# Optimization experiments

Measured on AMD Instinct MI355X. Metric: run time of the kernel, lower is better.

## Reference

```python
import jax, jax.numpy as jnp
import numpy as np

B, N, DIM = 4, 4096, 1024
HEADS, DFF, WIN = 16, 4096, 128
EPS = 1e-5


def _layernorm(x, w, b):
    mu = jnp.mean(x, axis=-1, keepdims=True)
    var = jnp.mean(jnp.square(x - mu), axis=-1, keepdims=True)
    return (x - mu) * jax.lax.rsqrt(var + EPS) * w + b


def _local_attention(q, k, v, window):
    # q,k,v: (B, h, N, d); non-causal, look_backward=1, look_forward=1
    Bq, h, n, d = q.shape
    nb = n // window
    scale = d ** -0.5
    q = q.reshape(Bq * h, nb, window, d) * scale
    k = k.reshape(Bq * h, nb, window, d)
    v = v.reshape(Bq * h, nb, window, d)

    def look_around(t):  # (BH, nb, w, d) -> (BH, nb, 3w, d)
        tp = jnp.pad(t, ((0, 0), (1, 1), (0, 0), (0, 0)))
        return jnp.concatenate([tp[:, :-2], tp[:, 1:-1], tp[:, 2:]], axis=2)

    kk = look_around(k)
    vv = look_around(v)

    # validity mask for out-of-range look-around buckets
    idx = jnp.arange(n).reshape(nb, window)
    idx_p = jnp.pad(idx, ((1, 1), (0, 0)), constant_values=-1)
    kidx = jnp.concatenate([idx_p[:-2], idx_p[1:-1], idx_p[2:]], axis=1)  # (nb, 3w)
    valid = (kidx >= 0)[None, :, None, :]  # (1, nb, 1, 3w)

    sim = jnp.einsum('bnid,bnjd->bnij', q, kk)  # (BH, nb, w, 3w)
    neg = jnp.finfo(sim.dtype).min
    sim = jnp.where(valid, sim, neg)
    attn = jax.nn.softmax(sim, axis=-1)
    out = jnp.einsum('bnij,bnjd->bnid', attn, vv)
    return out.reshape(Bq, h, n, d)


def setup_inputs() -> dict:
    key = jax.random.key(0)
    ks = jax.random.split(key, 8)
    w = lambda k, shape: jax.random.normal(k, shape, jnp.float32) * 0.02
    return {
        'x': jax.random.normal(ks[0], (B, N, DIM), jnp.float32),
        'ln1_w': jnp.ones((DIM,), jnp.float32), 'ln1_b': jnp.zeros((DIM,), jnp.float32),
        'qkv_w': w(ks[1], (3 * DIM, DIM)), 'qkv_b': jnp.zeros((3 * DIM,), jnp.float32),
        'proj_w': w(ks[2], (DIM, DIM)), 'proj_b': jnp.zeros((DIM,), jnp.float32),
        'ln2_w': jnp.ones((DIM,), jnp.float32), 'ln2_b': jnp.zeros((DIM,), jnp.float32),
        'fc1_w': w(ks[3], (DFF, DIM)), 'fc1_b': jnp.zeros((DFF,), jnp.float32),
        'fc2_w': w(ks[4], (DIM, DFF)), 'fc2_b': jnp.zeros((DIM,), jnp.float32),
    }


def reference(x, ln1_w, ln1_b, qkv_w, qkv_b, proj_w, proj_b, ln2_w, ln2_b, fc1_w, fc1_b, fc2_w, fc2_b):
    Bx, n, C = x.shape
    h = HEADS
    hd = C // h
    x_norm = _layernorm(x, ln1_w, ln1_b)
    qkv = x_norm @ qkv_w.T + qkv_b  # (B, N, 3C)
    qkv = qkv.reshape(Bx, n, 3, h, hd).transpose(2, 0, 3, 1, 4)  # (3, B, h, N, hd)
    q, k, v = qkv[0], qkv[1], qkv[2]
    attn_out = _local_attention(q, k, v, WIN)  # (B, h, N, hd)
    attn_out = attn_out.transpose(0, 2, 1, 3).reshape(Bx, n, C)
    x = x + (attn_out @ proj_w.T + proj_b)
    y = _layernorm(x, ln2_w, ln2_b)
    y = jax.nn.gelu(y @ fc1_w.T + fc1_b, approximate=False)
    x = x + (y @ fc2_w.T + fc2_b)
    return x
```

## Files before the change

kernel.cpp:

```cpp
#include <hip/hip_runtime.h>
#include <math.h>

typedef unsigned short u16;
typedef __attribute__((ext_vector_type(4))) float f32x4;
typedef __attribute__((ext_vector_type(8))) __bf16 bf16x8;
typedef __attribute__((ext_vector_type(8))) u16 u16x8;
typedef __attribute__((ext_vector_type(4))) u16 u16x4;

__device__ __forceinline__ float bf2f(u16 v) {
    unsigned int u = ((unsigned int)v) << 16;
    return __builtin_bit_cast(float, u);
}
__device__ __forceinline__ u16 f2bf(float f) {
    unsigned int x = __builtin_bit_cast(unsigned int, f);
    x += 0x7fffu + ((x >> 16) & 1u);
    return (u16)(x >> 16);
}

__device__ __forceinline__ void load_lds16(const u16* g, u16* l) {
    __builtin_amdgcn_global_load_lds((const __attribute__((address_space(1))) void*)g,
                                     (__attribute__((address_space(3))) void*)l, 16, 0, 0);
}

__global__ __launch_bounds__(256) void cvt_kernel(const float* __restrict__ in,
                                                  u16* __restrict__ out, int n)
{
    const int i = (blockIdx.x * 256 + threadIdx.x) * 4;
    if (i >= n) return;
    const float4 f = *(const float4*)(in + i);
    u16x4 o;
    o[0] = f2bf(f.x); o[1] = f2bf(f.y); o[2] = f2bf(f.z); o[3] = f2bf(f.w);
    *(u16x4*)(out + i) = o;
}

template<int EPI, int RES, bool OF32>
__global__ __launch_bounds__(256) void gemm_bt(
    const u16* __restrict__ A, const u16* __restrict__ W,
    const float* __restrict__ bias,
    const float* __restrict__ resf, const u16* __restrict__ resb,
    void* __restrict__ O0v, u16* __restrict__ O1, u16* __restrict__ O2,
    int M, int N, int K, int mbase)
{
    __shared__ u16 As[128 * 32];
    __shared__ u16 Bs[128 * 32];
    const int tid  = threadIdx.x;
    const int wave = tid >> 6;
    const int lane = tid & 63;
    const int m0   = blockIdx.y * 128;
    const int n0   = blockIdx.x * 128;
    const int wm   = (wave >> 1) * 64;
    const int wn   = (wave & 1) * 64;

    const int srow = lane >> 2;
    const int scol = (lane & 3) * 8;
    const u16* ag0 = A + (size_t)(m0 + wave * 16 + srow) * K + scol;
    const u16* ag1 = ag0 + (size_t)64 * K;
    const u16* bg0 = W + (size_t)(n0 + wave * 16 + srow) * K + scol;
    const u16* bg1 = bg0 + (size_t)64 * K;
    u16* as0 = As + (wave * 16) * 32;
    u16* as1 = As + (64 + wave * 16) * 32;
    u16* bs0 = Bs + (wave * 16) * 32;
    u16* bs1 = Bs + (64 + wave * 16) * 32;

    const int colq = lane & 15;
    const int quad = lane >> 4;

    f32x4 acc[4][4] = {};

    for (int k0 = 0; k0 < K; k0 += 32) {
        if (k0) __syncthreads();
        load_lds16(ag0 + k0, as0);
        load_lds16(ag1 + k0, as1);
        load_lds16(bg0 + k0, bs0);
        load_lds16(bg1 + k0, bs1);
        __syncthreads();
        bf16x8 a[4], b[4];
#pragma unroll
        for (int i = 0; i < 4; ++i) {
            a[i] = *(const bf16x8*)(As + (wm + i * 16 + colq) * 32 + quad * 8);
            b[i] = *(const bf16x8*)(Bs + (wn + i * 16 + colq) * 32 + quad * 8);
        }
#pragma unroll
        for (int mi = 0; mi < 4; ++mi)
#pragma unroll
            for (int ni = 0; ni < 4; ++ni)
                acc[mi][ni] = __builtin_amdgcn_mfma_f32_16x16x32_bf16(a[mi], b[ni], acc[mi][ni], 0, 0, 0);
    }

#pragma unroll
    for (int ni = 0; ni < 4; ++ni) {
        const int c = n0 + wn + ni * 16 + colq;
        const float bz = bias[c];
#pragma unroll
        for (int mi = 0; mi < 4; ++mi) {
#pragma unroll
            for (int i = 0; i < 4; ++i) {
                const int r = m0 + wm + mi * 16 + quad * 4 + i;
                float v = acc[mi][ni][i] + bz;
                if constexpr (EPI == 0) {
                    const int which = c >> 10;
                    const int head  = (c >> 6) & 15;
                    const int d     = c & 63;
                    const int rg    = mbase + r;
                    const int bb    = rg >> 12;
                    const int t     = rg & 4095;
                    const int bh    = bb * 16 + head;
                    const u16 val = f2bf(v);
                    if (which == 0)      ((u16*)O0v)[((size_t)bh * 4096 + t) * 64 + d] = val;
                    else if (which == 1) O1[((size_t)bh * 4096 + t) * 64 + d] = val;
                    else                 O2[((size_t)bh * 64 + d) * 4096 + t] = val;
                } else {
                    const size_t idx = (size_t)r * N + c;
                    if constexpr (RES == 1) v += resf[idx];
                    if constexpr (RES == 2) v += bf2f(resb[idx]);
                    if constexpr (EPI == 2) v = 0.5f * v * (1.0f + erff(v * 0.70710678118654752f));
                    if constexpr (OF32) ((float*)O0v)[idx] = v;
                    else                ((u16*)O0v)[idx] = f2bf(v);
                }
            }
        }
    }
}

template<bool F32IN>
__global__ __launch_bounds__(256) void ln_kernel(
    const void* __restrict__ xin, const float* __restrict__ w,
    const float* __restrict__ b, u16* __restrict__ out)
{
    const int wave = threadIdx.x >> 6, lane = threadIdx.x & 63;
    const size_t row = (size_t)blockIdx.x * 4 + wave;
    float v[16];
    if constexpr (F32IN) {
        const float* xr = (const float*)xin + row * 1024 + lane * 16;
#pragma unroll
        for (int j = 0; j < 4; ++j) {
            const float4 f = *(const float4*)(xr + j * 4);
            v[j * 4 + 0] = f.x; v[j * 4 + 1] = f.y; v[j * 4 + 2] = f.z; v[j * 4 + 3] = f.w;
        }
    } else {
        const u16* xr = (const u16*)xin + row * 1024 + lane * 16;
        u16x8 xa = *(const u16x8*)xr;
        u16x8 xb = *(const u16x8*)(xr + 8);
#pragma unroll
        for (int i = 0; i < 8; ++i) { v[i] = bf2f(xa[i]); v[8 + i] = bf2f(xb[i]); }
    }
    float s = 0.f, s2 = 0.f;
#pragma unroll
    for (int i = 0; i < 16; ++i) { s += v[i]; s2 += v[i] * v[i]; }
#pragma unroll
    for (int m = 32; m >= 1; m >>= 1) { s += __shfl_xor(s, m, 64); s2 += __shfl_xor(s2, m, 64); }
    const float mu  = s * (1.0f / 1024.0f);
    const float var = s2 * (1.0f / 1024.0f) - mu * mu;
    const float rs  = rsqrtf(var + 1e-5f);
    const float* wp = w + lane * 16;
    const float* bp = b + lane * 16;
    u16x8 oa, ob;
#pragma unroll
    for (int i = 0; i < 8; ++i) {
        oa[i] = f2bf((v[i]     - mu) * rs * wp[i]     + bp[i]);
        ob[i] = f2bf((v[8 + i] - mu) * rs * wp[8 + i] + bp[8 + i]);
    }
    u16* orow = out + row * 1024 + lane * 16;
    *(u16x8*)orow       = oa;
    *(u16x8*)(orow + 8) = ob;
}

__global__ __launch_bounds__(256, 4) void attn_kernel(
    const u16* __restrict__ Q, const u16* __restrict__ Kb,
    const u16* __restrict__ Vt, u16* __restrict__ out)
{
    __shared__ u16 Ps[4][16 * 200];
    const int tid  = threadIdx.x;
    const int wave = tid >> 6;
    const int lane = tid & 63;
    const int colq = lane & 15;
    const int quad = lane >> 4;

    const int f   = blockIdx.x;
    const int xcd = f & 7;
    const int s8  = f >> 3;
    const int bh  = s8 >> 3;
    const int tb  = (s8 & 7) + 8 * xcd;
    const int qrow0 = tb * 64 + wave * 16;
    const int nb    = tb >> 1;
    const int key0  = nb * 128 - 128;
    const int nt_lo = (nb == 0) ? 8 : 0;
    const int nt_hi = (nb == 31) ? 16 : 24;

    const u16* qp = Q + ((size_t)bh * 4096 + qrow0 + colq) * 64 + quad * 8;
    bf16x8 aq0 = *(const bf16x8*)qp;
    bf16x8 aq1 = *(const bf16x8*)(qp + 32);

    float m_i[4], l_i[4];
    f32x4 o[4] = {};
#pragma unroll
    for (int i = 0; i < 4; ++i) { m_i[i] = -3.0e38f; l_i[i] = 0.f; }

    u16* Psw = &Ps[wave][0];

#pragma unroll
    for (int c = 0; c < 2; ++c) {
        const int lo = (c == 0) ? nt_lo : 12;
        const int hi = (c == 0) ? ((nt_hi < 12) ? nt_hi : 12) : nt_hi;

        f32x4 sc[12];
#pragma unroll
        for (int j = 0; j < 12; ++j) sc[j] = (f32x4){0.f, 0.f, 0.f, 0.f};
#pragma unroll
        for (int j = 0; j < 12; ++j) {
            const int nt = c * 12 + j;
            if (nt >= lo && nt < hi) {
                const u16* kp = Kb + ((size_t)bh * 4096 + key0 + nt * 16 + colq) * 64 + quad * 8;
                bf16x8 b0 = *(const bf16x8*)kp;
                bf16x8 b1 = *(const bf16x8*)(kp + 32);
                f32x4 z = {0.f, 0.f, 0.f, 0.f};
                z = __builtin_amdgcn_mfma_f32_16x16x32_bf16(aq0, b0, z, 0, 0, 0);
                z = __builtin_amdgcn_mfma_f32_16x16x32_bf16(aq1, b1, z, 0, 0, 0);
                sc[j] = z;
            }
        }
        float mc[4];
#pragma unroll
        for (int i = 0; i < 4; ++i) mc[i] = -3.0e38f;
#pragma unroll
        for (int j = 0; j < 12; ++j) {
            const int nt = c * 12 + j;
            if (nt >= lo && nt < hi)
#pragma unroll
                for (int i = 0; i < 4; ++i) mc[i] = fmaxf(mc[i], sc[j][i]);
        }
#pragma unroll
        for (int i = 0; i < 4; ++i)
#pragma unroll
            for (int m = 8; m >= 1; m >>= 1) mc[i] = fmaxf(mc[i], __shfl_xor(mc[i], m, 64));
        float a_i[4], psum[4];
#pragma unroll
        for (int i = 0; i < 4; ++i) {
            const float mn = fmaxf(m_i[i], mc[i]);
            a_i[i] = __expf((m_i[i] - mn) * 0.125f);
            m_i[i] = mn;
            psum[i] = 0.f;
        }
#pragma unroll
        for (int j = 0; j < 12; ++j) {
            const int nt = c * 12 + j;
            if (nt >= lo && nt < hi) {
#pragma unroll
                for (int i = 0; i < 4; ++i) {
                    const float p = __expf((sc[j][i] - m_i[i]) * 0.125f);
                    psum[i] += p;
                    Psw[(quad * 4 + i) * 200 + j * 16 + colq] = f2bf(p);
                }
            }
        }
#pragma unroll
        for (int i = 0; i < 4; ++i)
#pragma unroll
            for (int m = 8; m >= 1; m >>= 1) psum[i] += __shfl_xor(psum[i], m, 64);
#pragma unroll
        for (int i = 0; i < 4; ++i) l_i[i] = l_i[i] * a_i[i] + psum[i];
#pragma unroll
        for (int dt = 0; dt < 4; ++dt)
#pragma unroll
            for (int i = 0; i < 4; ++i) o[dt][i] *= a_i[i];
        const int klo = (lo - c * 12) >> 1;
        const int khi = (hi - c * 12) >> 1;
#pragma unroll
        for (int k6 = 0; k6 < 6; ++k6) {
            if (k6 >= klo && k6 < khi) {
                bf16x8 ap = *(const bf16x8*)(Psw + colq * 200 + k6 * 32 + quad * 8);
                const int kk = key0 + (c * 6 + k6) * 32 + quad * 8;
#pragma unroll
                for (int dt = 0; dt < 4; ++dt) {
                    const u16* vp = Vt + ((size_t)bh * 64 + dt * 16 + colq) * 4096 + kk;
                    bf16x8 bv = *(const bf16x8*)vp;
                    o[dt] = __builtin_amdgcn_mfma_f32_16x16x32_bf16(ap, bv, o[dt], 0, 0, 0);
                }
            }
        }
    }

    const int bb = bh >> 4, hh = bh & 15;
#pragma unroll
    for (int i = 0; i < 4; ++i) {
        const float inv = 1.0f / fmaxf(l_i[i], 1e-20f);
        const int t = qrow0 + quad * 4 + i;
        u16* op = out + ((size_t)(bb * 4096 + t)) * 1024 + hh * 64;
#pragma unroll
        for (int dt = 0; dt < 4; ++dt) op[dt * 16 + colq] = f2bf(o[dt][i] * inv);
    }
}

extern "C" void kernel_launch(void* const* d_in, const int* in_sizes, int n_in,
                              void* d_out, int out_size, void* d_ws, size_t ws_size,
                              hipStream_t stream)
{
    const float* x      = (const float*)d_in[0];
    const float* ln1_w  = (const float*)d_in[1];
    const float* ln1_b  = (const float*)d_in[2];
    const float* qkv_w  = (const float*)d_in[3];
    const float* qkv_b  = (const float*)d_in[4];
    const float* proj_w = (const float*)d_in[5];
    const float* proj_b = (const float*)d_in[6];
    const float* ln2_w  = (const float*)d_in[7];
    const float* ln2_b  = (const float*)d_in[8];
    const float* fc1_w  = (const float*)d_in[9];
    const float* fc1_b  = (const float*)d_in[10];
    const float* fc2_w  = (const float*)d_in[11];
    const float* fc2_b  = (const float*)d_in[12];
    float* outp = (float*)d_out;

    if (ws_size < 134217728u) return;
    char* ws = (char*)d_ws;
    u16* R0 = (u16*)(ws);
    u16* R1 = (u16*)(ws + 33554432);
    u16* R2 = (u16*)(ws + 67108864);
    u16* R3 = (u16*)(ws + 100663296);
    u16* xnc    = (u16*)d_out;
    u16* attn_o = (u16*)((char*)d_out + 33554432);

    u16* qkvwb = R0;
    u16* projwb = R0 + 3145728;
    u16* fc1wb = R0 + 4194304;
    u16* fc2wb = R0 + 8388608;
    u16* Qb = R1, *Kb = R2, *Vtb = R3;
    u16* x2 = R1;
    u16* yn = attn_o;
    u16* hb = R2;

    cvt_kernel<<<3072, 256, 0, stream>>>(qkv_w, qkvwb, 3145728);
    cvt_kernel<<<1024, 256, 0, stream>>>(proj_w, projwb, 1048576);
    cvt_kernel<<<4096, 256, 0, stream>>>(fc1_w, fc1wb, 4194304);
    cvt_kernel<<<4096, 256, 0, stream>>>(fc2_w, fc2wb, 4194304);
    ln_kernel<true><<<4096, 256, 0, stream>>>(x, ln1_w, ln1_b, xnc);
    gemm_bt<0, 0, false><<<dim3(24, 128), 256, 0, stream>>>(xnc, qkvwb, qkv_b, nullptr, nullptr,
                                                            Qb, Kb, Vtb, 16384, 3072, 1024, 0);
    attn_kernel<<<4096, 256, 0, stream>>>(Qb, Kb, Vtb, attn_o);
    gemm_bt<1, 1, false><<<dim3(8, 128), 256, 0, stream>>>(attn_o, projwb, proj_b, x, nullptr,
                                                           x2, nullptr, nullptr, 16384, 1024, 1024, 0);
    ln_kernel<false><<<4096, 256, 0, stream>>>(x2, ln2_w, ln2_b, yn);
    for (int ci = 0; ci < 2; ++ci) {
        const size_t off = (size_t)ci * 8192 * 1024;
        gemm_bt<2, 0, false><<<dim3(32, 64), 256, 0, stream>>>(yn + off, fc1wb, fc1_b, nullptr, nullptr,
                                                               hb, nullptr, nullptr, 8192, 4096, 1024, 0);
        gemm_bt<1, 2, true><<<dim3(8, 64), 256, 0, stream>>>(hb, fc2wb, fc2_b, nullptr, x2 + off,
                                                             outp + off, nullptr, nullptr, 8192, 1024, 4096, 0);
    }
}
```

Baseline: 1.030 ms.

## Replace 128x128 GEMM with double-buffered 256x256 tile, swizzled LDS, phased MFMA schedule

Replaces the simple 128x128 single-buffered GEMM with a 512-thread 256x256 tile kernel. It uses double-buffered LDS (128KB), XOR-swizzled layout to avoid bank conflicts, and prefetch of the next K-tile interleaved across four MFMA phases with explicit vmcnt waits and barriers. It also remaps block IDs across the 8 XCDs for locality and raises MFMA priority with setprio. The intent is to raise arithmetic intensity and hide global-load latency in all four GEMMs. The cost is much higher LDS and register pressure and fewer blocks for the smaller GEMMs (e.g. 256 blocks for proj).

```diff
diff --git a/kernel.cpp b/kernel.cpp
--- a/kernel.cpp
+++ b/kernel.cpp
@@ -20,6 +20,17 @@
 __device__ __forceinline__ void load_lds16(const u16* g, u16* l) {
     __builtin_amdgcn_global_load_lds((const __attribute__((address_space(1))) void*)g,
                                      (__attribute__((address_space(3))) void*)l, 16, 0, 0);
+}
+
+#define WAIT_VM(N) asm volatile("s_waitcnt vmcnt(" #N ")" ::: "memory")
+#define MFMA16(d, x, y) d = __builtin_amdgcn_mfma_f32_16x16x32_bf16(x, y, d, 0, 0, 0)
+
+__device__ __forceinline__ void phase_barrier() {
+    __builtin_amdgcn_sched_barrier(0);
+    asm volatile("" ::: "memory");
+    __builtin_amdgcn_s_barrier();
+    asm volatile("" ::: "memory");
+    __builtin_amdgcn_sched_barrier(0);
 }
 
 __global__ __launch_bounds__(256) void cvt_kernel(const float* __restrict__ in,
@@ -34,81 +45,155 @@
 }
 
 template<int EPI, int RES, bool OF32>
-__global__ __launch_bounds__(256) void gemm_bt(
+__global__ __launch_bounds__(512, 2) void gemm256(
     const u16* __restrict__ A, const u16* __restrict__ W,
     const float* __restrict__ bias,
     const float* __restrict__ resf, const u16* __restrict__ resb,
     void* __restrict__ O0v, u16* __restrict__ O1, u16* __restrict__ O2,
     int M, int N, int K, int mbase)
 {
-    __shared__ u16 As[128 * 32];
-    __shared__ u16 Bs[128 * 32];
+    __shared__ u16 S[65536];
     const int tid  = threadIdx.x;
-    const int wave = tid >> 6;
-    const int lane = tid & 63;
-    const int m0   = blockIdx.y * 128;
-    const int n0   = blockIdx.x * 128;
-    const int wm   = (wave >> 1) * 64;
-    const int wn   = (wave & 1) * 64;
-
-    const int srow = lane >> 2;
-    const int scol = (lane & 3) * 8;
-    const u16* ag0 = A + (size_t)(m0 + wave * 16 + srow) * K + scol;
-    const u16* ag1 = ag0 + (size_t)64 * K;
-    const u16* bg0 = W + (size_t)(n0 + wave * 16 + srow) * K + scol;
-    const u16* bg1 = bg0 + (size_t)64 * K;
-    u16* as0 = As + (wave * 16) * 32;
-    u16* as1 = As + (64 + wave * 16) * 32;
-    u16* bs0 = Bs + (wave * 16) * 32;
-    u16* bs1 = Bs + (64 + wave * 16) * 32;
-
-    const int colq = lane & 15;
-    const int quad = lane >> 4;
-
-    f32x4 acc[4][4] = {};
-
-    for (int k0 = 0; k0 < K; k0 += 32) {
-        if (k0) __syncthreads();
-        load_lds16(ag0 + k0, as0);
-        load_lds16(ag1 + k0, as1);
-        load_lds16(bg0 + k0, bs0);
-        load_lds16(bg1 + k0, bs1);
-        __syncthreads();
-        bf16x8 a[4], b[4];
-#pragma unroll
-        for (int i = 0; i < 4; ++i) {
-            a[i] = *(const bf16x8*)(As + (wm + i * 16 + colq) * 32 + quad * 8);
-            b[i] = *(const bf16x8*)(Bs + (wn + i * 16 + colq) * 32 + quad * 8);
-        }
-#pragma unroll
-        for (int mi = 0; mi < 4; ++mi)
-#pragma unroll
-            for (int ni = 0; ni < 4; ++ni)
-                acc[mi][ni] = __builtin_amdgcn_mfma_f32_16x16x32_bf16(a[mi], b[ni], acc[mi][ni], 0, 0, 0);
-    }
-
-#pragma unroll
-    for (int ni = 0; ni < 4; ++ni) {
-        const int c = n0 + wn + ni * 16 + colq;
+    const int w    = tid >> 6;
+    const int l    = tid & 63;
+    const int colq = l & 15;
+    const int quad = l >> 4;
+    const int w3   = w & 3;
+    const int wm   = (w >> 2) * 128;
+    const int wn   = w3 * 64;
+
+    const int nX  = (int)gridDim.x;
+    const int nwg = nX * (int)gridDim.y;
+    const int did = (int)blockIdx.y * nX + (int)blockIdx.x;
+    const int q8  = nwg >> 3;
+    const int wg  = (nwg & 7) ? did : ((did & 7) * q8 + (did >> 3));
+    const int bm  = wg / nX;
+    const int bn  = wg - bm * nX;
+    const int m0  = bm * 256, n0 = bn * 256;
+
+    const int rw   = l >> 3;
+    const int sseg = ((l & 7) ^ rw) * 8;
+    const u16* gA[2][2];
+    const u16* gB[2][2];
+#pragma unroll
+    for (int h = 0; h < 2; ++h)
+#pragma unroll
+        for (int j = 0; j < 2; ++j) {
+            const int rr = (w * 2 + j) * 8 + rw;
+            gA[h][j] = A + (size_t)(m0 + h * 128 + rr) * K + sseg;
+            const int nl = (rr >> 5) * 64 + (h * 2 + ((rr >> 4) & 1)) * 16 + (rr & 15);
+            gB[h][j] = W + (size_t)(n0 + nl) * K + sseg;
+        }
+    const int lw = w * 1024;
+
+    const int c0   = (quad * 8) ^ ((colq & 7) << 3);
+    const int c1   = c0 ^ 32;
+    const int aoff = (wm + colq) * 64;
+    const int boff = 16384 + (w3 * 32 + colq) * 64;
+
+    f32x4 acc[8][4] = {};
+    bf16x8 a0[8], a1[8], b0, b1;
+
+#pragma unroll
+    for (int h = 0; h < 2; ++h)
+#pragma unroll
+        for (int j = 0; j < 2; ++j)
+            load_lds16(gA[h][j], S + h * 8192 + lw + j * 512);
+#pragma unroll
+    for (int h = 0; h < 2; ++h)
+#pragma unroll
+        for (int j = 0; j < 2; ++j)
+            load_lds16(gB[h][j], S + 16384 + h * 8192 + lw + j * 512);
+    WAIT_VM(2);
+    phase_barrier();
+
+    const int NT = K >> 6;
+    for (int t = 0; t < NT; ++t) {
+        u16* Sc = S + ((t & 1) << 15);
+        u16* Sn = S + (((t + 1) & 1) << 15);
+        const int  kk = (t + 1) << 6;
+        const bool pf = (t + 1) < NT;
+
+#pragma unroll
+        for (int mf = 0; mf < 8; ++mf)
+            a0[mf] = *(const bf16x8*)(Sc + aoff + mf * 1024 + c0);
+        b0 = *(const bf16x8*)(Sc + boff + c0);
+        b1 = *(const bf16x8*)(Sc + boff + 1024 + c0);
+        if (pf) {
+#pragma unroll
+            for (int h = 0; h < 2; ++h)
+#pragma unroll
+                for (int j = 0; j < 2; ++j)
+                    load_lds16(gA[h][j] + kk, Sn + h * 8192 + lw + j * 512);
+        }
+        __builtin_amdgcn_s_setprio(1);
+#pragma unroll
+        for (int mf = 0; mf < 8; ++mf) { MFMA16(acc[mf][0], a0[mf], b0); MFMA16(acc[mf][1], a0[mf], b1); }
+        __builtin_amdgcn_s_setprio(0);
+        phase_barrier();
+
+#pragma unroll
+        for (int mf = 0; mf < 8; ++mf)
+            a1[mf] = *(const bf16x8*)(Sc + aoff + mf * 1024 + c1);
+        b0 = *(const bf16x8*)(Sc + boff + c1);
+        b1 = *(const bf16x8*)(Sc + boff + 1024 + c1);
+        if (pf) {
+#pragma unroll
+            for (int j = 0; j < 2; ++j)
+                load_lds16(gB[0][j] + kk, Sn + 16384 + lw + j * 512);
+        }
+        __builtin_amdgcn_s_setprio(1);
+#pragma unroll
+        for (int mf = 0; mf < 8; ++mf) { MFMA16(acc[mf][0], a1[mf], b0); MFMA16(acc[mf][1], a1[mf], b1); }
+        __builtin_amdgcn_s_setprio(0);
+        if (pf) { WAIT_VM(6); } else { WAIT_VM(0); }
+        phase_barrier();
+
+        b0 = *(const bf16x8*)(Sc + boff + 8192 + c0);
+        b1 = *(const bf16x8*)(Sc + boff + 8192 + 1024 + c0);
+        if (pf) {
+#pragma unroll
+            for (int j = 0; j < 2; ++j)
+                load_lds16(gB[1][j] + kk, Sn + 16384 + 8192 + lw + j * 512);
+        }
+        __builtin_amdgcn_s_setprio(1);
+#pragma unroll
+        for (int mf = 0; mf < 8; ++mf) { MFMA16(acc[mf][2], a0[mf], b0); MFMA16(acc[mf][3], a0[mf], b1); }
+        __builtin_amdgcn_s_setprio(0);
+        phase_barrier();
+
+        b0 = *(const bf16x8*)(Sc + boff + 8192 + c1);
+        b1 = *(const bf16x8*)(Sc + boff + 8192 + 1024 + c1);
+        __builtin_amdgcn_s_setprio(1);
+#pragma unroll
+        for (int mf = 0; mf < 8; ++mf) { MFMA16(acc[mf][2], a1[mf], b0); MFMA16(acc[mf][3], a1[mf], b1); }
+        __builtin_amdgcn_s_setprio(0);
+        if (pf) { WAIT_VM(2); }
+        phase_barrier();
+    }
+
+#pragma unroll
+    for (int nf = 0; nf < 4; ++nf) {
+        const int c = n0 + wn + nf * 16 + colq;
         const float bz = bias[c];
 #pragma unroll
-        for (int mi = 0; mi < 4; ++mi) {
+        for (int mf = 0; mf < 8; ++mf) {
 #pragma unroll
             for (int i = 0; i < 4; ++i) {
-                const int r = m0 + wm + mi * 16 + quad * 4 + i;
-                float v = acc[mi][ni][i] + bz;
+                const int r = m0 + wm + mf * 16 + quad * 4 + i;
+                float v = acc[mf][nf][i] + bz;
                 if constexpr (EPI == 0) {
                     const int which = c >> 10;
                     const int head  = (c >> 6) & 15;
                     const int d     = c & 63;
                     const int rg    = mbase + r;
                     const int bb    = rg >> 12;
-                    const int t     = rg & 4095;
+                    const int tt    = rg & 4095;
                     const int bh    = bb * 16 + head;
                     const u16 val = f2bf(v);
-                    if (which == 0)      ((u16*)O0v)[((size_t)bh * 4096 + t) * 64 + d] = val;
-                    else if (which == 1) O1[((size_t)bh * 4096 + t) * 64 + d] = val;
-                    else                 O2[((size_t)bh * 64 + d) * 4096 + t] = val;
+                    if (which == 0)      ((u16*)O0v)[((size_t)bh * 4096 + tt) * 64 + d] = val;
+                    else if (which == 1) O1[((size_t)bh * 4096 + tt) * 64 + d] = val;
+                    else                 O2[((size_t)bh * 64 + d) * 4096 + tt] = val;
                 } else {
                     const size_t idx = (size_t)r * N + c;
                     if constexpr (RES == 1) v += resf[idx];
@@ -269,10 +354,10 @@
         for (int k6 = 0; k6 < 6; ++k6) {
             if (k6 >= klo && k6 < khi) {
                 bf16x8 ap = *(const bf16x8*)(Psw + colq * 200 + k6 * 32 + quad * 8);
-                const int kk = key0 + (c * 6 + k6) * 32 + quad * 8;
+                const int kkk = key0 + (c * 6 + k6) * 32 + quad * 8;
 #pragma unroll
                 for (int dt = 0; dt < 4; ++dt) {
-                    const u16* vp = Vt + ((size_t)bh * 64 + dt * 16 + colq) * 4096 + kk;
+                    const u16* vp = Vt + ((size_t)bh * 64 + dt * 16 + colq) * 4096 + kkk;
                     bf16x8 bv = *(const bf16x8*)vp;
                     o[dt] = __builtin_amdgcn_mfma_f32_16x16x32_bf16(ap, bv, o[dt], 0, 0, 0);
                 }
@@ -333,17 +418,17 @@
     cvt_kernel<<<4096, 256, 0, stream>>>(fc1_w, fc1wb, 4194304);
     cvt_kernel<<<4096, 256, 0, stream>>>(fc2_w, fc2wb, 4194304);
     ln_kernel<true><<<4096, 256, 0, stream>>>(x, ln1_w, ln1_b, xnc);
-    gemm_bt<0, 0, false><<<dim3(24, 128), 256, 0, stream>>>(xnc, qkvwb, qkv_b, nullptr, nullptr,
-                                                            Qb, Kb, Vtb, 16384, 3072, 1024, 0);
+    gemm256<0, 0, false><<<dim3(12, 64), 512, 0, stream>>>(xnc, qkvwb, qkv_b, nullptr, nullptr,
+                                                           Qb, Kb, Vtb, 16384, 3072, 1024, 0);
     attn_kernel<<<4096, 256, 0, stream>>>(Qb, Kb, Vtb, attn_o);
-    gemm_bt<1, 1, false><<<dim3(8, 128), 256, 0, stream>>>(attn_o, projwb, proj_b, x, nullptr,
-                                                           x2, nullptr, nullptr, 16384, 1024, 1024, 0);
+    gemm256<1, 1, false><<<dim3(4, 64), 512, 0, stream>>>(attn_o, projwb, proj_b, x, nullptr,
+                                                          x2, nullptr, nullptr, 16384, 1024, 1024, 0);
     ln_kernel<false><<<4096, 256, 0, stream>>>(x2, ln2_w, ln2_b, yn);
     for (int ci = 0; ci < 2; ++ci) {
         const size_t off = (size_t)ci * 8192 * 1024;
-        gemm_bt<2, 0, false><<<dim3(32, 64), 256, 0, stream>>>(yn + off, fc1wb, fc1_b, nullptr, nullptr,
+        gemm256<2, 0, false><<<dim3(16, 32), 512, 0, stream>>>(yn + off, fc1wb, fc1_b, nullptr, nullptr,
                                                                hb, nullptr, nullptr, 8192, 4096, 1024, 0);
-        gemm_bt<1, 2, true><<<dim3(8, 64), 256, 0, stream>>>(hb, fc2wb, fc2_b, nullptr, x2 + off,
+        gemm256<1, 2, true><<<dim3(4, 32), 512, 0, stream>>>(hb, fc2wb, fc2_b, nullptr, x2 + off,
                                                              outp + off, nullptr, nullptr, 8192, 1024, 4096, 0);
     }
 }
```

New measurement: 1.033 ms. About the same (+0.3%).
